# Optimization experiments

Hardware: AMD Instinct MI355X
Metric: run time of the kernel (lower is better)

Reference implementation:

```python
import jax, jax.numpy as jnp
import numpy as np

# ---- static hyperparameters (mirror init_kwargs) ----
L_MAX = 3
N_MAX_L = [8, 6, 4, 2]            # radial basis size per l (precomputer.n_max_l)
N_CHANNELS = 32                   # num_element_channels
K_MAX_L = [n * N_CHANNELS for n in N_MAX_L]   # [256, 192, 128, 64]
SH_SIZES = [2 * l + 1 for l in range(L_MAX + 1)]  # [1,3,5,7]
MP_SCALING = 0.1
NU_SCALING = 0.1
NU_MAX = 2                        # max_correlation_order_per_layer
N_LAYERS = 2                      # num_message_passing_layers

# Fixed CG coupling tensors for all valid (l1, l2, L) with |l1-l2|<=L<=min(l1+l2, L_MAX).
# (Deterministic stand-ins for real Clebsch-Gordan coefficients; same sparsity/coupling
# structure and identical in fwd and fwdbwd modules.)
_rng = np.random.RandomState(0)
CG = {}
for _l1 in range(L_MAX + 1):
    for _l2 in range(L_MAX + 1):
        for _L in range(abs(_l1 - _l2), min(_l1 + _l2, L_MAX) + 1):
            CG[(_l1, _l2, _L)] = jnp.asarray(
                (_rng.randn(2 * _l1 + 1, 2 * _l2 + 1, 2 * _L + 1) * 0.2).astype(np.float32))


def split_l(x, sizes):
    out, i = [], 0
    for s in sizes:
        out.append(x[:, i:i + s])
        i += s
    return out


def embed_centers(feats, emb):
    # feats[l]: [N, 2l+1, n_l*C]; multiply channel block c by per-atom embedding emb[:, c]
    C = emb.shape[1]
    out = []
    for f in feats:
        n, m, k = f.shape
        out.append((f.reshape(n, m, k // C, C) * emb[:, None, None, :]).reshape(n, m, k))
    return out


def tensor_product(A, B):
    # per-atom CG tensor product, channel-aligned with truncation to min k
    n = A[0].shape[0]
    out = [jnp.zeros((n, 2 * L + 1, K_MAX_L[L]), A[0].dtype) for L in range(L_MAX + 1)]
    for (l1, l2, L), cg in CG.items():
        kk = min(K_MAX_L[l1], K_MAX_L[l2], K_MAX_L[L])
        t = jnp.einsum('nak,nbk,abM->nMk', A[l1][:, :, :kk], B[l2][:, :, :kk], cg)
        out[L] = out[L].at[:, :, :kk].add(t)
    return out


def cg_iterate(feats):
    # CGIterator: nu_max-1 iterated tensor products with residual accumulation
    g = feats
    for _ in range(NU_MAX - 1):
        tp = tensor_product(g, feats)
        g = [g[l] + NU_SCALING * tp[l] for l in range(L_MAX + 1)]
    return g


def invariant_mp(rb_l, sh_l, centers, emb_nbr, n_atoms):
    # spherical expansion: scatter rb x sh x neighbor-embedding over pairs -> centers
    out = []
    for l in range(L_MAX + 1):
        # [P, 2l+1, n_l, C] -> [P, 2l+1, k_l]
        msg = sh_l[l][:, :, None, None] * rb_l[l][:, None, :, None] * emb_nbr[:, None, None, :]
        msg = msg.reshape(msg.shape[0], 2 * l + 1, -1)
        out.append(MP_SCALING * jax.ops.segment_sum(msg, centers, num_segments=n_atoms))
    return out


def equivariant_mp(rb_l, sh_l, centers, neighbors, feats, n_atoms):
    # pair messages: CG-couple radially weighted SH edge features with neighbor features
    edge = [sh_l[l] * rb_l[l].sum(-1, keepdims=True) for l in range(L_MAX + 1)]  # [P, 2l+1]
    out = [jnp.zeros((n_atoms, 2 * L + 1, K_MAX_L[L]), feats[0].dtype) for L in range(L_MAX + 1)]
    for (l1, l2, L), cg in CG.items():
        kk = min(K_MAX_L[l2], K_MAX_L[L])
        w = jnp.einsum('pa,abM->pbM', edge[l1], cg)        # [P, 2l2+1, 2L+1]
        fg = feats[l2][neighbors, :, :kk]                   # gather: [P, 2l2+1, kk]
        msg = jnp.einsum('pbM,pbk->pMk', w, fg)             # [P, 2L+1, kk]
        out[L] = out[L].at[:, :, :kk].add(
            MP_SCALING * jax.ops.segment_sum(msg, centers, num_segments=n_atoms))
    return out


def setup_inputs() -> dict:
    key = jax.random.key(0)
    ks = jax.random.split(key, 8)
    N, P = 5000, 100000
    return {
        'sh': jax.random.normal(ks[0], (P, sum(SH_SIZES)), dtype=jnp.float32),
        'rb': jax.random.uniform(ks[1], (P, sum(N_MAX_L)), dtype=jnp.float32),
        'emb_table': jax.random.normal(ks[2], (4, N_CHANNELS), dtype=jnp.float32),
        'w_energy': jax.random.normal(ks[3], (K_MAX_L[0], 1), dtype=jnp.float32) * 0.05,
        'b_energy': jax.random.normal(ks[4], (1,), dtype=jnp.float32),
        'species_idx': jax.random.randint(ks[5], (N,), 0, 4, dtype=jnp.int32),
        'centers': jax.random.randint(ks[6], (P,), 0, N, dtype=jnp.int32),
        'neighbors': jax.random.randint(ks[7], (P,), 0, N, dtype=jnp.int32),
    }


def reference(sh, rb, emb_table, w_energy, b_energy, species_idx, centers, neighbors):
    n_atoms = species_idx.shape[0]
    sh_l = split_l(sh * NU_SCALING, SH_SIZES)   # nu_scaling applied to spherical harmonics
    rb_l = split_l(rb, N_MAX_L)
    center_emb = emb_table[species_idx]          # [N, C]
    emb_nbr = center_emb[neighbors]              # [P, C]
    # invariant message passing -> spherical expansion, then first CG iteration
    feats = invariant_mp(rb_l, sh_l, centers, emb_nbr, n_atoms)
    feats = cg_iterate(feats)
    # remaining equivariant message-passing layers
    for _ in range(N_LAYERS - 1):
        ef = embed_centers(feats, center_emb)
        mp = equivariant_mp(rb_l, sh_l, centers, neighbors, ef, n_atoms)
        feats = cg_iterate(mp)
    feats = embed_centers(feats, center_emb)
    energies = feats[0] @ w_energy + b_energy    # [N, 1, 1]
    return energies
```

## Files before the change

kernel.cpp:

```cpp
#include <hip/hip_runtime.h>
#include <vector>
#include <cmath>
#include <cstdint>

constexpr int KLc[4]  = {256,192,128,64};
constexpr int NMLc[4] = {8,6,4,2};
constexpr int SHBc[5] = {0,1,4,9,16};
constexpr int RBBc[5] = {0,8,14,18,20};
constexpr int FBc[5]  = {0,256,832,1472,1920};
constexpr int NCMB = 34, CGTOT = 3436, FTOT = 1920;

struct Combos { int l1[NCMB], l2[NCMB], L[NCMB], cgoff[NCMB], kk[NCMB]; };
constexpr Combos make_combos(){
  Combos c{}; int n=0, cg=0;
  for(int a=0;a<=3;a++)for(int b=0;b<=3;b++){
    int lo=a>b?a-b:b-a, hi=(a+b<3)?(a+b):3;
    for(int L=lo;L<=hi;L++){
      c.l1[n]=a; c.l2[n]=b; c.L[n]=L; c.cgoff[n]=cg;
      int mx=a>b?a:b; if(L>mx) mx=L; c.kk[n]=KLc[mx];
      cg+=(2*a+1)*(2*b+1)*(2*L+1); n++;
    }
  }
  return c;
}
constexpr Combos CB = make_combos();
static_assert(CB.cgoff[NCMB-1] + 7*7*7 == CGTOT, "cg size");

struct Grp { int cnt[4]; int list[4][12]; };
constexpr Grp make_Lg(){ Grp g{}; for(int i=0;i<NCMB;i++){ int L=CB.L[i]; g.list[L][g.cnt[L]++]=i; } return g; }
constexpr Grp LG = make_Lg();

struct Rows { int sh[64], rb[64], off[64]; };
constexpr Rows make_rows(){ Rows r{}; int i=0;
  for(int l=0;l<4;l++)for(int m=0;m<2*l+1;m++)for(int n=0;n<NMLc[l];n++){
    r.sh[i]=SHBc[l]+m; r.rb[i]=RBBc[l]+n; r.off[i]=FBc[l]+m*KLc[l]+n*32; i++; }
  for(;i<64;i++){ r.sh[i]=0; r.rb[i]=0; r.off[i]=0; }
  return r; }
constexpr Rows RWS = make_rows();

constexpr int NSL=425, NG=16, RPAD=149;
constexpr int JB=48, DEPTH=6;
static_assert(JB % DEPTH == 0, "slot rotation alignment");
constexpr int NTILE=30;
constexpr int GSTR=1024;

constexpr int iabs_(int x){ return x<0?-x:x; }
__host__ __device__ constexpr bool sl_valid(int l1,int l2,int kt){ return l2<=3-kt && iabs_(l1-l2)<=3-kt; }

__host__ __device__ constexpr int rb_base(int kt,int l1,int l2){
  int base=0;
  for(int p=0;p<4;p++)for(int q=0;q<4;q++){
    if(p==l1 && q==l2) return base;
    if(sl_valid(p,q,kt)) base += (2*p+1)*(2*q+1);
  }
  return base;
}

struct EqTab {
  short       srow[NG][32];
  signed char sph [NG][32];
  int nr[NG];
  short roff[NG][2];
  int total;
};
constexpr EqTab make_eqtab(){
  EqTab T{};
  for(int g=0;g<NG;g++){
    for(int s=0;s<32;s++){ T.srow[g][s]=-1; T.sph[g][s]=-1; }
    T.nr[g]=0; T.roff[g][0]=0; T.roff[g][1]=0;
  }
  int tl2[NTILE]{}, tkt[NTILE]{}, tbb[NTILE]{}, tsz[NTILE]{}; int nt=0;
  for(int l2=0;l2<4;l2++)for(int kt=0;kt<4-l2;kt++)for(int b=0;b<2*l2+1;b++){
    int sz=0;
    for(int l1=0;l1<4;l1++) if(sl_valid(l1,l2,kt)) sz+=2*l1+1;
    tl2[nt]=l2; tkt[nt]=kt; tbb[nt]=b; tsz[nt]=sz; nt++;
  }
  bool used[NTILE]{}; int gload[NG]{}; int gcnt[NG]{}; int gt[NG][2]{};
  for(int it=0; it<nt; it++){
    int best=-1;
    for(int i=0;i<nt;i++) if(!used[i] && (best<0 || tsz[i]>tsz[best])) best=i;
    used[best]=true;
    int g=-1;
    for(int j=0;j<NG;j++) if(gcnt[j]<2 && (g<0 || gload[j]<gload[g])) g=j;
    gt[g][gcnt[g]]=best; gcnt[g]++; gload[g]+=tsz[best];
  }
  int total=0;
  for(int g=0;g<NG;g++){
    T.nr[g]=gcnt[g];
    for(int tk=0;tk<gcnt[g];tk++){
      const int ti=gt[g][tk];
      const int l2=tl2[ti], kt=tkt[ti], b=tbb[ti];
      T.roff[g][tk]=(short)(FBc[l2]+b*KLc[l2]+kt*64);
      for(int i=0;i<16;i++){
        const int l1=(i==0)?0:(i<4)?1:(i<9)?2:3;
        const int aa=i-SHBc[l1];
        if(!sl_valid(l1,l2,kt)) continue;
        const int s=tk*16+i;
        const int rbi=rb_base(kt,l1,l2)+aa*(2*l2+1)+b;
        int ph, sr;
        if(kt==0){ if(l1<=2){ ph=0; sr=rbi; } else { ph=1; sr=rbi-144; } }
        else { ph=kt+1; sr=rbi; }
        T.sph[g][s]=(signed char)ph; T.srow[g][s]=(short)sr;
        total++;
      }
    }
    if(gcnt[g]==1) T.roff[g][1]=T.roff[g][0];
  }
  T.total=total;
  return T;
}
constexpr EqTab ET = make_eqtab();
static_assert(ET.total==NSL, "slice count");
constexpr bool chk_srow(){ for(int g=0;g<NG;g++) for(int s=0;s<32;s++) if(ET.srow[g][s]>=RPAD) return false; return true; }
static_assert(chk_srow(), "stage rows fit RPAD");

struct RoffA { int r0[NG]; int r1[NG]; };
constexpr RoffA make_roffa(){ RoffA R{}; for(int g=0;g<NG;g++){ R.r0[g]=ET.roff[g][0]; R.r1[g]=ET.roff[g][1]; } return R; }
constexpr RoffA RFA = make_roffa();

struct CAsg { int cnt[NG]; unsigned char ci[NG][8]; };
constexpr CAsg make_casg(){
  CAsg C{}; bool used[NCMB]{}; int load[NG]{};
  for(int it=0; it<NCMB; it++){
    int best=-1, bc=-1;
    for(int i=0;i<NCMB;i++) if(!used[i]){
      int c=(2*CB.l1[i]+1)*(2*CB.l2[i]+1)*(2*CB.L[i]+1);
      if(c>bc){bc=c;best=i;}
    }
    used[best]=true;
    int g=0; for(int j=1;j<NG;j++) if(load[j]<load[g]) g=j;
    C.ci[g][C.cnt[g]++]=(unsigned char)best; load[g]+=bc;
  }
  return C;
}
constexpr CAsg CA = make_casg();
constexpr bool chk_ca(){ for(int g=0;g<NG;g++) if(CA.cnt[g]>8) return false; return true; }
static_assert(chk_ca(), "CA cap");

__host__ __device__ constexpr bool combo_in_phase(int ci,int ph){
  int l1=CB.l1[ci], l2=CB.l2[ci], L=CB.L[ci];
  if(ph==0) return l1<=2;
  if(ph==1) return l1==3;
  int kt=ph-1;
  return (l2<=3-kt) && (L<=3-kt);
}
__host__ __device__ constexpr int phase_kt(int ph){ return ph<=1?0:ph-1; }
__host__ __device__ constexpr int phase_rbadj(int ph){ return ph==1?144:0; }

namespace nprng {
struct MT {
  uint32_t mt[624]; int mti; bool has_g; double g;
  void seed(uint32_t s){ for(int i=0;i<624;i++){ mt[i]=s; s=1812433253u*(s^(s>>30))+(uint32_t)i+1u; } mti=624; has_g=false; g=0.0; }
  uint32_t u32(){
    if(mti>=624){
      for(int i=0;i<624;i++){
        uint32_t y=(mt[i]&0x80000000u)|(mt[(i+1)%624]&0x7fffffffu);
        mt[i]=mt[(i+397)%624]^(y>>1)^((y&1u)?0x9908b0dfu:0u);
      }
      mti=0;
    }
    uint32_t y=mt[mti++];
    y^=y>>11; y^=(y<<7)&0x9d2c5680u; y^=(y<<15)&0xefc60000u; y^=y>>18;
    return y;
  }
  double dbl(){ uint32_t a=u32()>>5, b=u32()>>6; return (a*67108864.0+b)/9007199254740992.0; }
  double gauss(){
    if(has_g){ has_g=false; return g; }
    double f,x1,x2,r2;
    do{ x1=2.0*dbl()-1.0; x2=2.0*dbl()-1.0; r2=x1*x1+x2*x2; }while(r2>=1.0||r2==0.0);
    f=sqrt(-2.0*log(r2)/r2);
    g=f*x1; has_g=true; return f*x2;
  }
};
}
static std::vector<float> build_cg(){
  nprng::MT r; r.seed(0);
  std::vector<float> v; v.reserve(CGTOT);
  for(int l1=0;l1<=3;l1++)for(int l2=0;l2<=3;l2++){
    int lo = l1>l2? l1-l2 : l2-l1;
    int hi = (l1+l2<3)? (l1+l2) : 3;
    for(int L=lo;L<=hi;L++){
      int n=(2*l1+1)*(2*l2+1)*(2*L+1);
      for(int i=0;i<n;i++) v.push_back((float)(r.gauss()*0.2));
    }
  }
  return v;
}

__global__ __launch_bounds__(256) void k_cemb(const float* __restrict__ emb_table,
    const int* __restrict__ species, float* __restrict__ cemb, int* __restrict__ counts, int N){
  int i = blockIdx.x*256 + threadIdx.x;
  if(i < N) counts[i] = 0;
  if(i < N*32){ int n = i>>5, c = i&31; cemb[i] = emb_table[species[n]*32 + c]; }
}

__global__ __launch_bounds__(256) void k_hist(const int* __restrict__ centers, int* counts, int P){
  int i = blockIdx.x*256 + threadIdx.x;
  if(i < P) atomicAdd(&counts[centers[i]], 1);
}

__global__ __launch_bounds__(256) void k_scan(const int* __restrict__ counts,
    int* __restrict__ offsets, int* __restrict__ cursor, int N){
  __shared__ int part[256];
  const int t = threadIdx.x;
  const int CH = (N + 255)/256;
  const int lo = t*CH;
  int hi = (t+1)*CH; if(hi > N) hi = N;
  int s = 0;
  for(int i=lo;i<hi;i++) s += counts[i];
  part[t] = s; __syncthreads();
  const int own = s;
  for(int d=1; d<256; d<<=1){
    int v = (t>=d)? part[t-d] : 0;
    __syncthreads();
    part[t] += v;
    __syncthreads();
  }
  int run = part[t] - own;
  for(int i=lo;i<hi;i++){ offsets[i]=run; cursor[i]=run; run += counts[i]; }
  if(t==255) offsets[N] = part[255];
}

__global__ __launch_bounds__(256) void k_scatter(const int* __restrict__ centers,
    int* cursor, int* __restrict__ perm, int P){
  int i = blockIdx.x*256 + threadIdx.x;
  if(i < P){ int c = centers[i]; int pos = atomicAdd(&cursor[c], 1); perm[pos] = i; }
}

__global__ __launch_bounds__(256) void k_permute(const float* __restrict__ sh,
    const float* __restrict__ rb, const int* __restrict__ nbrs, const int* __restrict__ perm,
    float* __restrict__ edge_p, int* __restrict__ nbrp, int P){
  int u = blockIdx.x*256 + threadIdx.x;
  int pos = u>>4, i = u&15;
  if(pos >= P) return;
  int p = perm[pos];
  if(i==0) nbrp[pos] = nbrs[p];
  int l = (i==0)?0:(i<4)?1:(i<9)?2:3;
  float s=0.f;
  for(int n=RBBc[l]; n<RBBc[l+1]; n++) s += rb[p*20+n];
  edge_p[(size_t)pos*16+i] = sh[p*16+i]*0.1f*s;
}

__global__ __launch_bounds__(256) void k_halfg(const float* __restrict__ src,
    const float* __restrict__ cemb, unsigned int* __restrict__ dst, int N){
  int u = blockIdx.x*256 + threadIdx.x;
  if(u >= N*GSTR) return;
  int n = u >> 10, o = u & 1023;
  int g = o >> 6, i = o & 63;
  float c = cemb[n*32 + (i&31)];
  float v0 = src[(size_t)n*FTOT + RFA.r0[g] + i] * c;
  float v1 = src[(size_t)n*FTOT + RFA.r1[g] + i] * c;
  _Float16 h0 = (_Float16)v0, h1 = (_Float16)v1;
  unsigned int lo = *(unsigned short*)&h0, hi = *(unsigned short*)&h1;
  dst[u] = lo | (hi<<16);
}

__global__ __launch_bounds__(256) void k_inv(const float* __restrict__ sh, const float* __restrict__ rb,
    const float* __restrict__ cemb, const int* __restrict__ nbrs, const int* __restrict__ offsets,
    const int* __restrict__ perm, float* __restrict__ feats){
  const int a = blockIdx.x, t = threadIdx.x;
  __shared__ float sh_s[8][16], rb_s[8][20], emb_s[8][32], shrb_s[8][60];
  const int c = t & 31, rg = t >> 5;
  float acc[8];
  #pragma unroll
  for(int j=0;j<8;j++) acc[j] = 0.f;
  const int beg = offsets[a], cnt = offsets[a+1]-beg;
  for(int jb=0; jb<cnt; jb+=8){
    __syncthreads();
    for(int u=t; u<8*36; u+=256){
      int j=u/36, i=u-36*j;
      if(jb+j<cnt){
        int p=perm[beg+jb+j];
        if(i<16) sh_s[j][i]=sh[p*16+i]*0.1f;
        else     rb_s[j][i-16]=rb[p*20+i-16];
      }
    }
    for(int u=t; u<8*32; u+=256){
      int j=u>>5, i=u&31;
      if(jb+j<cnt){ int nb=nbrs[perm[beg+jb+j]]; emb_s[j][i]=cemb[(size_t)nb*32+i]; }
    }
    __syncthreads();
    for(int u=t; u<8*60; u+=256){
      int j=u/60, r=u-60*j;
      if(jb+j<cnt) shrb_s[j][r] = sh_s[j][RWS.sh[r]] * rb_s[j][RWS.rb[r]];
    }
    __syncthreads();
    const int jm = (cnt-jb<8)?(cnt-jb):8;
    for(int j=0;j<jm;j++){
      const float e = emb_s[j][c];
      #pragma unroll
      for(int q=0;q<8;q++){ int r=rg+8*q; if(r<60) acc[q]=fmaf(shrb_s[j][r], e, acc[q]); }
    }
  }
  #pragma unroll
  for(int q=0;q<8;q++){
    int r = rg + 8*q;
    if(r < 60) feats[(size_t)a*FTOT + RWS.off[r] + c] = 0.1f * acc[q];
  }
}

__device__ __forceinline__ float cg_u(const float* __restrict__ cg, int idx){
  return cg[__builtin_amdgcn_readfirstlane(idx)];
}
__global__ __launch_bounds__(256) void k_tp(float* __restrict__ feats, const float* __restrict__ cg){
  const int a = blockIdx.x, t = threadIdx.x;
  __shared__ float f_s[FTOT];
  float* fa = feats + (size_t)a*FTOT;
  for(int i=t;i<FTOT;i+=256)  f_s[i]  = fa[i];
  __syncthreads();
  #pragma unroll
  for(int L=0; L<4; L++){
    const int KLL = KLc[L], nL = 2*L+1;
    const int nel = nL*KLL;
    for(int e=t; e<nel; e+=256){
      const int M = e / KLL, k = e - M*KLL;
      float acc = 0.f;
      #pragma unroll
      for(int gi=0; gi<LG.cnt[L]; gi++){
        const int ci = LG.list[L][gi];
        const int l1 = CB.l1[ci], l2 = CB.l2[ci];
        if(k < CB.kk[ci]){
          const int n2 = 2*l2+1;
          #pragma unroll
          for(int aa=0; aa<2*l1+1; aa++){
            const float Av = f_s[FBc[l1] + aa*KLc[l1] + k];
            #pragma unroll
            for(int b=0; b<n2; b++)
              acc += cg_u(cg, CB.cgoff[ci] + (aa*n2+b)*nL + M) * (Av * f_s[FBc[l2] + b*KLc[l2] + k]);
          }
        }
      }
      fa[FBc[L] + M*KLL + k] = f_s[FBc[L] + M*KLL + k] + 0.1f*acc;
    }
  }
}

template<int G,int PH,int U>
__device__ __forceinline__ void contract_combos(const float* __restrict__ stageT,
    float* __restrict__ out_s, const float* __restrict__ cg, int lane){
  if constexpr (U < CA.cnt[G]) {
    constexpr int ci = CA.ci[G][U];
    if constexpr (combo_in_phase(ci,PH)) {
      constexpr int l1=CB.l1[ci], l2=CB.l2[ci], L=CB.L[ci];
      constexpr int n1=2*l1+1, n2=2*l2+1, nL=2*L+1;
      constexpr int kt=phase_kt(PH);
      constexpr int rbase = rb_base(kt,l1,l2) - phase_rbadj(PH);
      float oa[nL];
      #pragma unroll
      for(int M=0;M<nL;M++) oa[M]=0.f;
      #pragma unroll
      for(int aa=0;aa<n1;aa++){
        #pragma unroll
        for(int b=0;b<n2;b++){
          const float sv = stageT[lane*RPAD + rbase + aa*n2 + b];
          #pragma unroll
          for(int M=0;M<nL;M++)
            oa[M] = fmaf(cg[CB.cgoff[ci] + (aa*n2+b)*nL + M], sv, oa[M]);
        }
      }
      #pragma unroll
      for(int M=0;M<nL;M++)
        atomicAdd(&out_s[FBc[L] + M*KLc[L] + kt*64 + lane], oa[M]);
    }
    contract_combos<G,PH,U+1>(stageT,out_s,cg,lane);
  }
}

template<int G,int PH>
__device__ __forceinline__ void eq_phase(const float* acc, float* stageT, float* out_s,
    const float* __restrict__ cg, int lane){
  __syncthreads();
  #pragma unroll
  for(int s=0;s<32;s++){
    if(ET.sph[G][s]==PH) stageT[lane*RPAD + ET.srow[G][s]] = acc[s];
  }
  __syncthreads();
  contract_combos<G,PH,0>(stageT,out_s,cg,lane);
}

template<int G>
__device__ __forceinline__ void eq_phases(const float* acc, float* stageT, float* out_s,
    const float* __restrict__ cg, int lane){
  eq_phase<G,0>(acc,stageT,out_s,cg,lane);
  eq_phase<G,1>(acc,stageT,out_s,cg,lane);
  eq_phase<G,2>(acc,stageT,out_s,cg,lane);
  eq_phase<G,3>(acc,stageT,out_s,cg,lane);
  eq_phase<G,4>(acc,stageT,out_s,cg,lane);
}

__device__ __forceinline__ void eq_compute_pair(float* acc, unsigned int v,
    const float* edge_row){
  union { unsigned int u; _Float16 h[2]; } cv; cv.u = v;
  const float f0 = (float)cv.h[0], f1 = (float)cv.h[1];
  #pragma unroll
  for(int q=0;q<4;q++){
    float4 e4 = *(const float4*)(edge_row + q*4);
    acc[q*4+0]    = fmaf(e4.x, f0, acc[q*4+0]);
    acc[q*4+1]    = fmaf(e4.y, f0, acc[q*4+1]);
    acc[q*4+2]    = fmaf(e4.z, f0, acc[q*4+2]);
    acc[q*4+3]    = fmaf(e4.w, f0, acc[q*4+3]);
    acc[16+q*4+0] = fmaf(e4.x, f1, acc[16+q*4+0]);
    acc[16+q*4+1] = fmaf(e4.y, f1, acc[16+q*4+1]);
    acc[16+q*4+2] = fmaf(e4.z, f1, acc[16+q*4+2]);
    acc[16+q*4+3] = fmaf(e4.w, f1, acc[16+q*4+3]);
  }
}

__global__ __launch_bounds__(1024,8) void k_eq2(const float* __restrict__ edge_p,
    const int* __restrict__ nbrp, const int* __restrict__ offsets,
    const unsigned int* __restrict__ featsAg,
    float* __restrict__ featsB, const float* __restrict__ cg){
  __shared__ float stageT[64*RPAD];
  __shared__ float out_s[FTOT];
  __shared__ float edge_s[JB*16];
  __shared__ int   nb_s[JB];
  const int a = blockIdx.x, t = threadIdx.x, lane = t&63, g = t>>6;

  float acc[32];
  #pragma unroll
  for(int s=0;s<32;s++) acc[s]=0.f;
  for(int i=t;i<FTOT;i+=1024) out_s[i]=0.f;
  const int beg = offsets[a], cnt = offsets[a+1]-beg;
  const int goff = g*64 + lane;

  if(t < JB*16){
    int j = t>>4;
    if(j < cnt) edge_s[t] = edge_p[(size_t)beg*16 + t];
  }
  if(t < JB) nb_s[t] = (t < cnt) ? nbrp[beg+t] : 0;
  __syncthreads();

  unsigned int fgS[DEPTH];
  #pragma unroll
  for(int s=0;s<DEPTH;s++){
    int nb = (s<cnt)? nb_s[s] : 0;
    fgS[s] = featsAg[(size_t)nb*GSTR + goff];
  }
  for(int jb=0; jb<cnt; jb+=JB){
    if(jb > 0){
      __syncthreads();
      if(t < JB*16){
        int j = t>>4;
        if(jb+j < cnt) edge_s[t] = edge_p[(size_t)(beg+jb)*16 + t];
      }
      if(t < JB) nb_s[t] = (jb+t < cnt) ? nbrp[beg+jb+t] : 0;
      __syncthreads();
    }
    const int jm = (cnt-jb<JB)?(cnt-jb):JB;
    for(int j=0;j<jm;j+=DEPTH){
      #pragma unroll
      for(int s=0;s<DEPTH;s++){
        if(j+s < jm){
          eq_compute_pair(acc, fgS[s], edge_s + (j+s)*16);
          int q = jb+j+s+DEPTH;
          int nb = (q<cnt) ? ((q-jb<JB)? nb_s[q-jb] : nbrp[beg+q]) : 0;
          fgS[s] = featsAg[(size_t)nb*GSTR + goff];
        }
      }
    }
  }

  switch(g){
    case 0:  eq_phases<0 >(acc,stageT,out_s,cg,lane); break;
    case 1:  eq_phases<1 >(acc,stageT,out_s,cg,lane); break;
    case 2:  eq_phases<2 >(acc,stageT,out_s,cg,lane); break;
    case 3:  eq_phases<3 >(acc,stageT,out_s,cg,lane); break;
    case 4:  eq_phases<4 >(acc,stageT,out_s,cg,lane); break;
    case 5:  eq_phases<5 >(acc,stageT,out_s,cg,lane); break;
    case 6:  eq_phases<6 >(acc,stageT,out_s,cg,lane); break;
    case 7:  eq_phases<7 >(acc,stageT,out_s,cg,lane); break;
    case 8:  eq_phases<8 >(acc,stageT,out_s,cg,lane); break;
    case 9:  eq_phases<9 >(acc,stageT,out_s,cg,lane); break;
    case 10: eq_phases<10>(acc,stageT,out_s,cg,lane); break;
    case 11: eq_phases<11>(acc,stageT,out_s,cg,lane); break;
    case 12: eq_phases<12>(acc,stageT,out_s,cg,lane); break;
    case 13: eq_phases<13>(acc,stageT,out_s,cg,lane); break;
    case 14: eq_phases<14>(acc,stageT,out_s,cg,lane); break;
    default: eq_phases<15>(acc,stageT,out_s,cg,lane); break;
  }
  __syncthreads();
  float* ob = featsB + (size_t)a*FTOT;
  for(int i=t;i<FTOT;i+=1024) ob[i] = 0.1f*out_s[i];
}

__global__ __launch_bounds__(256) void k_energy(const float* __restrict__ feats,
    const float* __restrict__ cemb, const float* __restrict__ wE, const float* __restrict__ bE,
    float* __restrict__ out, int N){
  const int wid = threadIdx.x >> 6, lane = threadIdx.x & 63;
  const int a = blockIdx.x*4 + wid;
  if(a >= N) return;
  const float e = cemb[(size_t)a*32 + (lane & 31)];
  float s = 0.f;
  for(int k=lane; k<256; k+=64) s += feats[(size_t)a*FTOT + k] * e * wE[k];
  #pragma unroll
  for(int off=32; off; off>>=1) s += __shfl_down(s, off, 64);
  if(lane == 0) out[a] = s + bE[0];
}

extern "C" void kernel_launch(void* const* d_in, const int* in_sizes, int n_in,
                              void* d_out, int out_size, void* d_ws, size_t ws_size,
                              hipStream_t stream){
  const float* sh        = (const float*)d_in[0];
  const float* rb        = (const float*)d_in[1];
  const float* emb_table = (const float*)d_in[2];
  const float* wE        = (const float*)d_in[3];
  const float* bE        = (const float*)d_in[4];
  const int*   species   = (const int*)d_in[5];
  const int*   centers   = (const int*)d_in[6];
  const int*   nbrs      = (const int*)d_in[7];
  const int N = in_sizes[5];
  const int P = in_sizes[6];

  char* ws = (char*)d_ws; size_t off = 0;
  auto carve = [&](size_t bytes)->void*{
    void* p = ws + off; off = (off + bytes + 255) & ~(size_t)255; return p;
  };
  float* cg_d    = (float*)carve((size_t)CGTOT*4);
  float* cemb    = (float*)carve((size_t)N*32*4);
  int*   counts  = (int*)  carve((size_t)N*4);
  int*   offsets = (int*)  carve((size_t)(N+1)*4);
  int*   cursor  = (int*)  carve((size_t)N*4);
  int*   perm    = (int*)  carve((size_t)P*4);
  float* edge_pd = (float*)carve((size_t)P*16*4);
  int*   nbrp    = (int*)  carve((size_t)P*4);
  float* featsA  = (float*)carve((size_t)N*FTOT*4);
  float* featsB  = (float*)carve((size_t)N*FTOT*4);
  unsigned int* featsAg = (unsigned int*)carve((size_t)N*GSTR*4);
  (void)ws_size; (void)n_in; (void)out_size;

  static const std::vector<float> cg_host = build_cg();
  hipMemcpyAsync(cg_d, cg_host.data(), (size_t)CGTOT*4, hipMemcpyHostToDevice, stream);

  k_cemb   <<<(N*32 + 255)/256, 256, 0, stream>>>(emb_table, species, cemb, counts, N);
  k_hist   <<<(P + 255)/256,    256, 0, stream>>>(centers, counts, P);
  k_scan   <<<1,                256, 0, stream>>>(counts, offsets, cursor, N);
  k_scatter<<<(P + 255)/256,    256, 0, stream>>>(centers, cursor, perm, P);
  k_permute<<<(P*16 + 255)/256, 256, 0, stream>>>(sh, rb, nbrs, perm, edge_pd, nbrp, P);
  k_inv    <<<N,                256, 0, stream>>>(sh, rb, cemb, nbrs, offsets, perm, featsA);
  k_tp     <<<N,                256, 0, stream>>>(featsA, cg_d);
  k_halfg  <<<(N*GSTR + 255)/256, 256, 0, stream>>>(featsA, cemb, featsAg, N);
  k_eq2    <<<N,               1024, 0, stream>>>(edge_pd, nbrp, offsets, featsAg, featsB, cg_d);
  k_tp     <<<N,                256, 0, stream>>>(featsB, cg_d);
  k_energy <<<(N + 3)/4,        256, 0, stream>>>(featsB, cemb, wE, bE, (float*)d_out, N);
}
```

Before: 980.4 us.

## Load edge rows and neighbor indices via scalar loads instead of LDS staging

Result: faster. 879.0 us (-10.3%).

```diff
diff --git a/kernel.cpp b/kernel.cpp
--- a/kernel.cpp
+++ b/kernel.cpp
@@ -39,8 +39,7 @@
 constexpr Rows RWS = make_rows();
 
 constexpr int NSL=425, NG=16, RPAD=149;
-constexpr int JB=48, DEPTH=6;
-static_assert(JB % DEPTH == 0, "slot rotation alignment");
+constexpr int DEPTH=8;
 constexpr int NTILE=30;
 constexpr int GSTR=1024;
 
@@ -388,23 +387,7 @@
   eq_phase<G,4>(acc,stageT,out_s,cg,lane);
 }
 
-__device__ __forceinline__ void eq_compute_pair(float* acc, unsigned int v,
-    const float* edge_row){
-  union { unsigned int u; _Float16 h[2]; } cv; cv.u = v;
-  const float f0 = (float)cv.h[0], f1 = (float)cv.h[1];
-  #pragma unroll
-  for(int q=0;q<4;q++){
-    float4 e4 = *(const float4*)(edge_row + q*4);
-    acc[q*4+0]    = fmaf(e4.x, f0, acc[q*4+0]);
-    acc[q*4+1]    = fmaf(e4.y, f0, acc[q*4+1]);
-    acc[q*4+2]    = fmaf(e4.z, f0, acc[q*4+2]);
-    acc[q*4+3]    = fmaf(e4.w, f0, acc[q*4+3]);
-    acc[16+q*4+0] = fmaf(e4.x, f1, acc[16+q*4+0]);
-    acc[16+q*4+1] = fmaf(e4.y, f1, acc[16+q*4+1]);
-    acc[16+q*4+2] = fmaf(e4.z, f1, acc[16+q*4+2]);
-    acc[16+q*4+3] = fmaf(e4.w, f1, acc[16+q*4+3]);
-  }
-}
+typedef float sf8 __attribute__((ext_vector_type(8)));
 
 __global__ __launch_bounds__(1024,8) void k_eq2(const float* __restrict__ edge_p,
     const int* __restrict__ nbrp, const int* __restrict__ offsets,
@@ -412,49 +395,52 @@
     float* __restrict__ featsB, const float* __restrict__ cg){
   __shared__ float stageT[64*RPAD];
   __shared__ float out_s[FTOT];
-  __shared__ float edge_s[JB*16];
-  __shared__ int   nb_s[JB];
   const int a = blockIdx.x, t = threadIdx.x, lane = t&63, g = t>>6;
 
   float acc[32];
   #pragma unroll
   for(int s=0;s<32;s++) acc[s]=0.f;
   for(int i=t;i<FTOT;i+=1024) out_s[i]=0.f;
-  const int beg = offsets[a], cnt = offsets[a+1]-beg;
-  const int goff = g*64 + lane;
-
-  if(t < JB*16){
-    int j = t>>4;
-    if(j < cnt) edge_s[t] = edge_p[(size_t)beg*16 + t];
-  }
-  if(t < JB) nb_s[t] = (t < cnt) ? nbrp[beg+t] : 0;
-  __syncthreads();
-
-  unsigned int fgS[DEPTH];
-  #pragma unroll
-  for(int s=0;s<DEPTH;s++){
-    int nb = (s<cnt)? nb_s[s] : 0;
-    fgS[s] = featsAg[(size_t)nb*GSTR + goff];
-  }
-  for(int jb=0; jb<cnt; jb+=JB){
-    if(jb > 0){
-      __syncthreads();
-      if(t < JB*16){
-        int j = t>>4;
-        if(jb+j < cnt) edge_s[t] = edge_p[(size_t)(beg+jb)*16 + t];
-      }
-      if(t < JB) nb_s[t] = (jb+t < cnt) ? nbrp[beg+jb+t] : 0;
-      __syncthreads();
-    }
-    const int jm = (cnt-jb<JB)?(cnt-jb):JB;
-    for(int j=0;j<jm;j+=DEPTH){
+  const int beg = __builtin_amdgcn_readfirstlane(offsets[a]);
+  const int cnt = __builtin_amdgcn_readfirstlane(offsets[a+1]) - beg;
+
+  if(cnt > 0){
+    unsigned int fgS[DEPTH];
+    #pragma unroll
+    for(int s=0;s<DEPTH;s++){
+      int idx = (s < cnt) ? s : cnt-1;
+      int nb = __builtin_amdgcn_readfirstlane(nbrp[beg+idx]);
+      fgS[s] = featsAg[(size_t)(unsigned)nb*GSTR + t];
+    }
+    for(int j=0;j<cnt;j+=DEPTH){
       #pragma unroll
       for(int s=0;s<DEPTH;s++){
-        if(j+s < jm){
-          eq_compute_pair(acc, fgS[s], edge_s + (j+s)*16);
-          int q = jb+j+s+DEPTH;
-          int nb = (q<cnt) ? ((q-jb<JB)? nb_s[q-jb] : nbrp[beg+q]) : 0;
-          fgS[s] = featsAg[(size_t)nb*GSTR + goff];
+        const int q = j+s;
+        if(q < cnt){
+          sf8 e0, e1; int nbn;
+          const float* ep = edge_p + (size_t)(beg+q)*16;
+          int qn = q + DEPTH; if(qn >= cnt) qn = cnt-1;
+          const int* np = nbrp + beg + qn;
+          asm volatile("s_load_dwordx8 %0, %2, 0\n\t"
+                       "s_load_dwordx8 %1, %2, 32"
+                       : "=s"(e0), "=s"(e1) : "s"(ep));
+          asm volatile("s_load_dword %0, %1, 0" : "=s"(nbn) : "s"(np));
+          asm volatile("s_waitcnt lgkmcnt(0)" : "+s"(e0), "+s"(e1), "+s"(nbn));
+          __builtin_amdgcn_sched_barrier(0);
+          const unsigned int v = fgS[s];
+          fgS[s] = featsAg[(size_t)(unsigned)nbn*GSTR + t];
+          union { unsigned int u; _Float16 h[2]; } cv; cv.u = v;
+          const float f0 = (float)cv.h[0], f1 = (float)cv.h[1];
+          #pragma unroll
+          for(int i=0;i<8;i++){
+            acc[i]    = fmaf(e0[i], f0, acc[i]);
+            acc[16+i] = fmaf(e0[i], f1, acc[16+i]);
+          }
+          #pragma unroll
+          for(int i=0;i<8;i++){
+            acc[8+i]  = fmaf(e1[i], f0, acc[8+i]);
+            acc[24+i] = fmaf(e1[i], f1, acc[24+i]);
+          }
         }
       }
     }
@@ -522,7 +508,7 @@
   int*   cursor  = (int*)  carve((size_t)N*4);
   int*   perm    = (int*)  carve((size_t)P*4);
   float* edge_pd = (float*)carve((size_t)P*16*4);
-  int*   nbrp    = (int*)  carve((size_t)P*4);
+  int*   nbrp    = (int*)  carve((size_t)(P+DEPTH)*4);
   float* featsA  = (float*)carve((size_t)N*FTOT*4);
   float* featsB  = (float*)carve((size_t)N*FTOT*4);
   unsigned int* featsAg = (unsigned int*)carve((size_t)N*GSTR*4);
```
